# Kernel tuning notes

Hardware: AMD Instinct MI355X
Metric: run time of the kernel (lower is better)

The kernel has to match this reference:

```python
import jax, jax.numpy as jnp
import numpy as np

B, N, E, H = 32, 512, 256, 8
HD = E // H
EPS = 1e-5

def setup_inputs() -> dict:
    key = jax.random.key(0)
    ks = jax.random.split(key, 10)
    x = jax.random.normal(ks[0], (B, N, E), dtype=jnp.float32)
    # boolean masks: True = masked out. Keep diagonal unmasked so no row is fully masked.
    pre = jax.random.bernoulli(ks[1], 0.1, (B, H, N, N))
    eye = jnp.eye(N, dtype=bool)
    pre_mask = jnp.where(eye[None, None, :, :], False, pre)
    post_attn_mask = jax.random.bernoulli(ks[2], 0.1, (B, N))
    s = 1.0 / np.sqrt(E)
    in_proj_w = jax.random.uniform(ks[3], (3 * E, E), jnp.float32, -s, s)
    in_proj_b = jnp.zeros((3 * E,), jnp.float32)
    out_w = jax.random.uniform(ks[4], (E, E), jnp.float32, -s, s)
    out_b = jnp.zeros((E,), jnp.float32)
    gamma = jnp.ones((E,), jnp.float32)
    beta = jnp.zeros((E,), jnp.float32)
    return {"x": x, "pre_mask": pre_mask, "post_attn_mask": post_attn_mask,
            "in_proj_w": in_proj_w, "in_proj_b": in_proj_b,
            "out_w": out_w, "out_b": out_b, "gamma": gamma, "beta": beta}

def reference(x, pre_mask, post_attn_mask, in_proj_w, in_proj_b, out_w, out_b, gamma, beta):
    b, n, e = x.shape
    # fused qkv projection (matches nn.MultiheadAttention in_proj)
    qkv = x @ in_proj_w.T + in_proj_b            # [B,N,3E]
    q, k, v = jnp.split(qkv, 3, axis=-1)
    def heads(t):
        return t.reshape(b, n, H, HD).transpose(0, 2, 1, 3)  # [B,H,N,HD]
    q, k, v = heads(q), heads(k), heads(v)
    scores = jnp.einsum('bhqd,bhkd->bhqk', q * (HD ** -0.5), k)  # [B,H,N,N]
    scores = jnp.where(pre_mask, -1e9, scores)
    w = jax.nn.softmax(scores, axis=-1)                          # [B,H,N,N]
    o = jnp.einsum('bhqk,bhkd->bhqd', w, v)                      # [B,H,N,HD]
    o = o.transpose(0, 2, 1, 3).reshape(b, n, e)
    o = o @ out_w.T + out_b
    # post-attention mask: zero outputs of unavailable agents
    o = jnp.where(post_attn_mask[:, :, None], 0.0, o)
    # residual + LayerNorm
    y = x + o
    mu = y.mean(axis=-1, keepdims=True)
    var = y.var(axis=-1, keepdims=True)
    out = (y - mu) * jax.lax.rsqrt(var + EPS) * gamma + beta
    # attn_weights averaged over heads (PyTorch default average_attn_weights=True)
    attn_weights = w.mean(axis=1)                                # [B,N,N]
    return (out, attn_weights)
```

## Files before the change

### kernel.cpp

```cpp
#include <hip/hip_runtime.h>

#define BB 32
#define NN 512
#define EE 256
#define HH 8
#define HDD 32

typedef __attribute__((ext_vector_type(4))) float f32x4;
typedef __attribute__((ext_vector_type(8))) short s16x8;
typedef unsigned short ushort_t;
typedef unsigned int uint_t;

__device__ __forceinline__ ushort_t f2bf(float f) {
  union { float f; uint_t u; } v; v.f = f;
  uint_t r = v.u + 0x7fffu + ((v.u >> 16) & 1u);
  return (ushort_t)(r >> 16);
}
__device__ __forceinline__ uint_t pk2(float a, float b) {
  return (uint_t)f2bf(a) | ((uint_t)f2bf(b) << 16);
}

__global__ __launch_bounds__(256) void qkv_mfma(
    const float* __restrict__ x, const float* __restrict__ w,
    const float* __restrict__ bias,
    ushort_t* __restrict__ Q, ushort_t* __restrict__ K, ushort_t* __restrict__ V) {
  __shared__ ushort_t sA[128][40];
  __shared__ ushort_t sB[128][40];
  int t = threadIdx.x;
  int bj = blockIdx.x % 6, bm = blockIdx.x / 6;
  int m0 = bm * 128, j0 = bj * 128;
  int w4 = t >> 6, lane = t & 63, quad = lane >> 4, l16 = lane & 15;
  int wy = w4 >> 1, wx = w4 & 1;
  f32x4 acc[4][4];
  #pragma unroll
  for (int a = 0; a < 4; a++)
    #pragma unroll
    for (int b = 0; b < 4; b++) acc[a][b] = (f32x4){0.f, 0.f, 0.f, 0.f};
  int sr = t >> 3, sc = t & 7;
  for (int kk = 0; kk < 256; kk += 32) {
    __syncthreads();
    #pragma unroll
    for (int i = 0; i < 4; i++) {
      int r = sr + 32 * i;
      float4 av = *(const float4*)&x[(size_t)(m0 + r) * 256 + kk + sc * 4];
      float4 bv = *(const float4*)&w[(size_t)(j0 + r) * 256 + kk + sc * 4];
      uint2 pa; pa.x = pk2(av.x, av.y); pa.y = pk2(av.z, av.w);
      uint2 pb; pb.x = pk2(bv.x, bv.y); pb.y = pk2(bv.z, bv.w);
      *(uint2*)&sA[r][sc * 4] = pa;
      *(uint2*)&sB[r][sc * 4] = pb;
    }
    __syncthreads();
    s16x8 af[4], bf[4];
    #pragma unroll
    for (int mt = 0; mt < 4; mt++)
      af[mt] = *(const s16x8*)&sA[wy * 64 + mt * 16 + l16][quad * 8];
    #pragma unroll
    for (int jt = 0; jt < 4; jt++)
      bf[jt] = *(const s16x8*)&sB[wx * 64 + jt * 16 + l16][quad * 8];
    #pragma unroll
    for (int mt = 0; mt < 4; mt++)
      #pragma unroll
      for (int jt = 0; jt < 4; jt++)
        acc[mt][jt] = __builtin_amdgcn_mfma_f32_16x16x32_bf16(af[mt], bf[jt], acc[mt][jt], 0, 0, 0);
  }
  #pragma unroll
  for (int jt = 0; jt < 4; jt++) {
    int j = j0 + wx * 64 + jt * 16 + l16;
    int which = j >> 8, e0 = j & 255, h = e0 >> 5, d0 = e0 & 31;
    ushort_t* dst = (which == 0) ? Q : ((which == 1) ? K : V);
    float b = bias[j];
    #pragma unroll
    for (int mt = 0; mt < 4; mt++) {
      #pragma unroll
      for (int r = 0; r < 4; r++) {
        int m = m0 + wy * 64 + mt * 16 + quad * 4 + r;
        int bi = m >> 9, n = m & 511;
        dst[((size_t)(bi * 8 + h) * 512 + n) * 32 + d0] = f2bf(acc[mt][jt][r] + b);
      }
    }
  }
}

__global__ __launch_bounds__(256) void attn_kernel(
    const ushort_t* __restrict__ Q, const ushort_t* __restrict__ K,
    const ushort_t* __restrict__ V, const int* __restrict__ pre_mask,
    ushort_t* __restrict__ O, float* __restrict__ attnw) {
  __shared__ ushort_t sQ[16 * 32];
  __shared__ ushort_t sP[16 * 520];
  __shared__ float sSum[4][16];
  __shared__ float sO[4][16 * 32];

  int t = threadIdx.x;
  int bb = blockIdx.x >> 5;
  int q0 = (blockIdx.x & 31) << 4;
  int w = t >> 6;
  int lane = t & 63;
  int quad = lane >> 4;
  int l16 = lane & 15;
  int kbase = w * 128;
  const float scale = 0.17677669529663687f;

  float wmean[4][8];
  #pragma unroll
  for (int i = 0; i < 4; i++)
    #pragma unroll
    for (int j = 0; j < 8; j++) wmean[i][j] = 0.f;

  for (int h = 0; h < 8; h++) {
    size_t base = ((size_t)(bb * 8 + h) * 512) * 32;
    const ushort_t* Kg = K + base;
    const ushort_t* Vg = V + base;
    const int* mbase = pre_mask + ((size_t)(bb * 8 + h) * 512 + q0) * 512;

    if (t < 64) {
      ((s16x8*)sQ)[t] = ((const s16x8*)(Q + base + (size_t)q0 * 32))[t];
    }
    __syncthreads();

    s16x8 afrag = *(const s16x8*)&sQ[l16 * 32 + quad * 8];
    float ev[8][4];
    #pragma unroll
    for (int t8 = 0; t8 < 8; t8++) {
      int n0 = kbase + t8 * 16;
      s16x8 bfrag = *(const s16x8*)&Kg[(size_t)(n0 + l16) * 32 + quad * 8];
      f32x4 acc = {0.f, 0.f, 0.f, 0.f};
      acc = __builtin_amdgcn_mfma_f32_16x16x32_bf16(afrag, bfrag, acc, 0, 0, 0);
      #pragma unroll
      for (int i = 0; i < 4; i++) {
        int msk = mbase[(quad * 4 + i) * 512 + n0 + l16];
        ev[t8][i] = msk ? 0.f : __expf(acc[i] * scale);
      }
    }
    float ps[4];
    #pragma unroll
    for (int i = 0; i < 4; i++) {
      float s = 0.f;
      #pragma unroll
      for (int t8 = 0; t8 < 8; t8++) s += ev[t8][i];
      s += __shfl_xor(s, 1, 64);
      s += __shfl_xor(s, 2, 64);
      s += __shfl_xor(s, 4, 64);
      s += __shfl_xor(s, 8, 64);
      ps[i] = s;
    }
    if (l16 == 0) {
      #pragma unroll
      for (int i = 0; i < 4; i++) sSum[w][quad * 4 + i] = ps[i];
    }
    #pragma unroll
    for (int t8 = 0; t8 < 8; t8++)
      #pragma unroll
      for (int i = 0; i < 4; i++)
        sP[(quad * 4 + i) * 520 + kbase + t8 * 16 + l16] = f2bf(ev[t8][i]);
    __syncthreads();

    float inv[4];
    #pragma unroll
    for (int i = 0; i < 4; i++) {
      int r = quad * 4 + i;
      inv[i] = 1.0f / (sSum[0][r] + sSum[1][r] + sSum[2][r] + sSum[3][r]);
    }
    #pragma unroll
    for (int t8 = 0; t8 < 8; t8++)
      #pragma unroll
      for (int i = 0; i < 4; i++)
        wmean[i][t8] += 0.125f * ev[t8][i] * inv[i];

    f32x4 oacc[2];
    oacc[0] = (f32x4){0.f, 0.f, 0.f, 0.f};
    oacc[1] = (f32x4){0.f, 0.f, 0.f, 0.f};
    #pragma unroll
    for (int ks = 0; ks < 4; ks++) {
      s16x8 pa = *(const s16x8*)&sP[l16 * 520 + kbase + ks * 32 + quad * 8];
      #pragma unroll
      for (int dt = 0; dt < 2; dt++) {
        s16x8 vb;
        #pragma unroll
        for (int j = 0; j < 8; j++)
          vb[j] = (short)Vg[(size_t)(kbase + ks * 32 + quad * 8 + j) * 32 + dt * 16 + l16];
        oacc[dt] = __builtin_amdgcn_mfma_f32_16x16x32_bf16(pa, vb, oacc[dt], 0, 0, 0);
      }
    }
    #pragma unroll
    for (int dt = 0; dt < 2; dt++)
      #pragma unroll
      for (int i = 0; i < 4; i++)
        sO[w][(quad * 4 + i) * 32 + dt * 16 + l16] = oacc[dt][i];
    __syncthreads();

    {
      int r = t >> 4;
      int c = (t & 15) * 2;
      float s0 = sO[0][r * 32 + c] + sO[1][r * 32 + c] + sO[2][r * 32 + c] + sO[3][r * 32 + c];
      float s1 = sO[0][r * 32 + c + 1] + sO[1][r * 32 + c + 1] + sO[2][r * 32 + c + 1] + sO[3][r * 32 + c + 1];
      float invr = 1.0f / (sSum[0][r] + sSum[1][r] + sSum[2][r] + sSum[3][r]);
      uint_t pk = pk2(s0 * invr, s1 * invr);
      *(uint_t*)&O[((size_t)(bb * 512 + q0 + r) * 256) + h * 32 + c] = pk;
    }
  }

  float* arow = attnw + (size_t)(bb * 512 + q0) * 512;
  #pragma unroll
  for (int i = 0; i < 4; i++)
    #pragma unroll
    for (int t8 = 0; t8 < 8; t8++)
      arow[(quad * 4 + i) * 512 + kbase + t8 * 16 + l16] = wmean[i][t8];
}

__global__ __launch_bounds__(256) void proj_ln_mfma(
    const ushort_t* __restrict__ O, const float* __restrict__ x,
    const float* __restrict__ w, const float* __restrict__ bias,
    const int* __restrict__ post_mask,
    const float* __restrict__ gamma, const float* __restrict__ beta,
    float* __restrict__ out) {
  __shared__ ushort_t sB[256][40];
  int t = threadIdx.x;
  int m0 = blockIdx.x * 64;
  int w4 = t >> 6, lane = t & 63, quad = lane >> 4, l16 = lane & 15;
  int mrow0 = m0 + w4 * 16;
  f32x4 acc[16];
  #pragma unroll
  for (int jt = 0; jt < 16; jt++) acc[jt] = (f32x4){0.f, 0.f, 0.f, 0.f};
  int sr = t >> 3, sc = t & 7;
  for (int kk = 0; kk < 256; kk += 32) {
    __syncthreads();
    #pragma unroll
    for (int i = 0; i < 8; i++) {
      int r = sr + 32 * i;
      float4 bv = *(const float4*)&w[(size_t)r * 256 + kk + sc * 4];
      uint2 pb; pb.x = pk2(bv.x, bv.y); pb.y = pk2(bv.z, bv.w);
      *(uint2*)&sB[r][sc * 4] = pb;
    }
    __syncthreads();
    s16x8 af = *(const s16x8*)&O[(size_t)(mrow0 + l16) * 256 + kk + quad * 8];
    #pragma unroll
    for (int jt = 0; jt < 16; jt++) {
      s16x8 bf = *(const s16x8*)&sB[jt * 16 + l16][quad * 8];
      acc[jt] = __builtin_amdgcn_mfma_f32_16x16x32_bf16(af, bf, acc[jt], 0, 0, 0);
    }
  }
  #pragma unroll
  for (int i = 0; i < 4; i++) {
    int m = mrow0 + quad * 4 + i;
    int bi = m >> 9, n = m & 511;
    bool msk = post_mask[bi * 512 + n] != 0;
    float y[16];
    float s1 = 0.f, s2 = 0.f;
    #pragma unroll
    for (int jt = 0; jt < 16; jt++) {
      int j = jt * 16 + l16;
      float p = msk ? 0.f : (acc[jt][i] + bias[j]);
      float yy = x[(size_t)m * 256 + j] + p;
      y[jt] = yy; s1 += yy; s2 += yy * yy;
    }
    s1 += __shfl_xor(s1, 1, 64); s1 += __shfl_xor(s1, 2, 64);
    s1 += __shfl_xor(s1, 4, 64); s1 += __shfl_xor(s1, 8, 64);
    s2 += __shfl_xor(s2, 1, 64); s2 += __shfl_xor(s2, 2, 64);
    s2 += __shfl_xor(s2, 4, 64); s2 += __shfl_xor(s2, 8, 64);
    float mu = s1 * (1.0f / 256.0f);
    float var = s2 * (1.0f / 256.0f) - mu * mu;
    float rstd = rsqrtf(var + 1e-5f);
    #pragma unroll
    for (int jt = 0; jt < 16; jt++) {
      int j = jt * 16 + l16;
      out[(size_t)m * 256 + j] = (y[jt] - mu) * rstd * gamma[j] + beta[j];
    }
  }
}

extern "C" void kernel_launch(void* const* d_in, const int* in_sizes, int n_in,
                              void* d_out, int out_size, void* d_ws, size_t ws_size,
                              hipStream_t stream) {
  const float* x       = (const float*)d_in[0];
  const int*   pre_m   = (const int*)d_in[1];
  const int*   post_m  = (const int*)d_in[2];
  const float* in_w    = (const float*)d_in[3];
  const float* in_b    = (const float*)d_in[4];
  const float* out_w   = (const float*)d_in[5];
  const float* out_b   = (const float*)d_in[6];
  const float* gamma   = (const float*)d_in[7];
  const float* beta    = (const float*)d_in[8];
  float* out   = (float*)d_out;
  float* attnw = out + (size_t)BB * NN * EE;
  ushort_t* Q = (ushort_t*)d_ws;
  ushort_t* K = Q + (size_t)BB * HH * NN * HDD;
  ushort_t* V = K + (size_t)BB * HH * NN * HDD;
  ushort_t* O = V + (size_t)BB * HH * NN * HDD;

  qkv_mfma<<<dim3(768), dim3(256), 0, stream>>>(x, in_w, in_b, Q, K, V);
  attn_kernel<<<dim3(1024), dim3(256), 0, stream>>>(Q, K, V, pre_m, O, attnw);
  proj_ln_mfma<<<dim3(256), dim3(256), 0, stream>>>(O, x, out_w, out_b, post_m, gamma, beta, out);
}
```

Before: 503.6 us.

## Pre-convert inputs to bf16 and store V transposed for vectorized PV loads

Adds a conversion kernel that turns x and both weight matrices into bf16 once, so the GEMM kernels load 16-byte bf16 vectors instead of converting fp32 per tile. The QKV kernel now writes V transposed (head-dim major), which lets the attention kernel load each V fragment with one 16-byte read instead of eight strided scalar reads. The cost is three extra launches, additional workspace traffic for the bf16 copies, and more scattered stores when writing V transposed.

```diff
diff --git a/kernel.cpp b/kernel.cpp
--- a/kernel.cpp
+++ b/kernel.cpp
@@ -20,10 +20,20 @@
   return (uint_t)f2bf(a) | ((uint_t)f2bf(b) << 16);
 }
 
+__global__ __launch_bounds__(256) void cvt_bf16(
+    const float* __restrict__ src, ushort_t* __restrict__ dst, int n4) {
+  int i = blockIdx.x * 256 + threadIdx.x;
+  if (i < n4) {
+    float4 v = ((const float4*)src)[i];
+    uint2 p; p.x = pk2(v.x, v.y); p.y = pk2(v.z, v.w);
+    ((uint2*)dst)[i] = p;
+  }
+}
+
 __global__ __launch_bounds__(256) void qkv_mfma(
-    const float* __restrict__ x, const float* __restrict__ w,
+    const ushort_t* __restrict__ xb, const ushort_t* __restrict__ wb,
     const float* __restrict__ bias,
-    ushort_t* __restrict__ Q, ushort_t* __restrict__ K, ushort_t* __restrict__ V) {
+    ushort_t* __restrict__ Q, ushort_t* __restrict__ K, ushort_t* __restrict__ Vt) {
   __shared__ ushort_t sA[128][40];
   __shared__ ushort_t sB[128][40];
   int t = threadIdx.x;
@@ -36,18 +46,14 @@
   for (int a = 0; a < 4; a++)
     #pragma unroll
     for (int b = 0; b < 4; b++) acc[a][b] = (f32x4){0.f, 0.f, 0.f, 0.f};
-  int sr = t >> 3, sc = t & 7;
+  int sr2 = t >> 2, sc2 = (t & 3) * 8;
   for (int kk = 0; kk < 256; kk += 32) {
     __syncthreads();
     #pragma unroll
-    for (int i = 0; i < 4; i++) {
-      int r = sr + 32 * i;
-      float4 av = *(const float4*)&x[(size_t)(m0 + r) * 256 + kk + sc * 4];
-      float4 bv = *(const float4*)&w[(size_t)(j0 + r) * 256 + kk + sc * 4];
-      uint2 pa; pa.x = pk2(av.x, av.y); pa.y = pk2(av.z, av.w);
-      uint2 pb; pb.x = pk2(bv.x, bv.y); pb.y = pk2(bv.z, bv.w);
-      *(uint2*)&sA[r][sc * 4] = pa;
-      *(uint2*)&sB[r][sc * 4] = pb;
+    for (int p = 0; p < 2; p++) {
+      int r = sr2 + 64 * p;
+      *(s16x8*)&sA[r][sc2] = *(const s16x8*)&xb[(size_t)(m0 + r) * 256 + kk + sc2];
+      *(s16x8*)&sB[r][sc2] = *(const s16x8*)&wb[(size_t)(j0 + r) * 256 + kk + sc2];
     }
     __syncthreads();
     s16x8 af[4], bf[4];
@@ -67,7 +73,6 @@
   for (int jt = 0; jt < 4; jt++) {
     int j = j0 + wx * 64 + jt * 16 + l16;
     int which = j >> 8, e0 = j & 255, h = e0 >> 5, d0 = e0 & 31;
-    ushort_t* dst = (which == 0) ? Q : ((which == 1) ? K : V);
     float b = bias[j];
     #pragma unroll
     for (int mt = 0; mt < 4; mt++) {
@@ -75,7 +80,13 @@
       for (int r = 0; r < 4; r++) {
         int m = m0 + wy * 64 + mt * 16 + quad * 4 + r;
         int bi = m >> 9, n = m & 511;
-        dst[((size_t)(bi * 8 + h) * 512 + n) * 32 + d0] = f2bf(acc[mt][jt][r] + b);
+        ushort_t val = f2bf(acc[mt][jt][r] + b);
+        if (which == 2) {
+          Vt[((size_t)(bi * 8 + h) * 32 + d0) * 512 + n] = val;
+        } else {
+          ushort_t* dst = (which == 0) ? Q : K;
+          dst[((size_t)(bi * 8 + h) * 512 + n) * 32 + d0] = val;
+        }
       }
     }
   }
@@ -83,7 +94,7 @@
 
 __global__ __launch_bounds__(256) void attn_kernel(
     const ushort_t* __restrict__ Q, const ushort_t* __restrict__ K,
-    const ushort_t* __restrict__ V, const int* __restrict__ pre_mask,
+    const ushort_t* __restrict__ Vt, const int* __restrict__ pre_mask,
     ushort_t* __restrict__ O, float* __restrict__ attnw) {
   __shared__ ushort_t sQ[16 * 32];
   __shared__ ushort_t sP[16 * 520];
@@ -109,7 +120,7 @@
   for (int h = 0; h < 8; h++) {
     size_t base = ((size_t)(bb * 8 + h) * 512) * 32;
     const ushort_t* Kg = K + base;
-    const ushort_t* Vg = V + base;
+    const ushort_t* Vg = Vt + base;
     const int* mbase = pre_mask + ((size_t)(bb * 8 + h) * 512 + q0) * 512;
 
     if (t < 64) {
@@ -174,10 +185,7 @@
       s16x8 pa = *(const s16x8*)&sP[l16 * 520 + kbase + ks * 32 + quad * 8];
       #pragma unroll
       for (int dt = 0; dt < 2; dt++) {
-        s16x8 vb;
-        #pragma unroll
-        for (int j = 0; j < 8; j++)
-          vb[j] = (short)Vg[(size_t)(kbase + ks * 32 + quad * 8 + j) * 32 + dt * 16 + l16];
+        s16x8 vb = *(const s16x8*)&Vg[(size_t)(dt * 16 + l16) * 512 + kbase + ks * 32 + quad * 8];
         oacc[dt] = __builtin_amdgcn_mfma_f32_16x16x32_bf16(pa, vb, oacc[dt], 0, 0, 0);
       }
     }
@@ -209,7 +217,7 @@
 
 __global__ __launch_bounds__(256) void proj_ln_mfma(
     const ushort_t* __restrict__ O, const float* __restrict__ x,
-    const float* __restrict__ w, const float* __restrict__ bias,
+    const ushort_t* __restrict__ wb, const float* __restrict__ bias,
     const int* __restrict__ post_mask,
     const float* __restrict__ gamma, const float* __restrict__ beta,
     float* __restrict__ out) {
@@ -221,15 +229,13 @@
   f32x4 acc[16];
   #pragma unroll
   for (int jt = 0; jt < 16; jt++) acc[jt] = (f32x4){0.f, 0.f, 0.f, 0.f};
-  int sr = t >> 3, sc = t & 7;
+  int sr2 = t >> 2, sc2 = (t & 3) * 8;
   for (int kk = 0; kk < 256; kk += 32) {
     __syncthreads();
     #pragma unroll
-    for (int i = 0; i < 8; i++) {
-      int r = sr + 32 * i;
-      float4 bv = *(const float4*)&w[(size_t)r * 256 + kk + sc * 4];
-      uint2 pb; pb.x = pk2(bv.x, bv.y); pb.y = pk2(bv.z, bv.w);
-      *(uint2*)&sB[r][sc * 4] = pb;
+    for (int p = 0; p < 4; p++) {
+      int r = sr2 + 64 * p;
+      *(s16x8*)&sB[r][sc2] = *(const s16x8*)&wb[(size_t)r * 256 + kk + sc2];
     }
     __syncthreads();
     s16x8 af = *(const s16x8*)&O[(size_t)(mrow0 + l16) * 256 + kk + quad * 8];
@@ -282,12 +288,18 @@
   const float* beta    = (const float*)d_in[8];
   float* out   = (float*)d_out;
   float* attnw = out + (size_t)BB * NN * EE;
-  ushort_t* Q = (ushort_t*)d_ws;
-  ushort_t* K = Q + (size_t)BB * HH * NN * HDD;
-  ushort_t* V = K + (size_t)BB * HH * NN * HDD;
-  ushort_t* O = V + (size_t)BB * HH * NN * HDD;
-
-  qkv_mfma<<<dim3(768), dim3(256), 0, stream>>>(x, in_w, in_b, Q, K, V);
-  attn_kernel<<<dim3(1024), dim3(256), 0, stream>>>(Q, K, V, pre_m, O, attnw);
-  proj_ln_mfma<<<dim3(256), dim3(256), 0, stream>>>(O, x, out_w, out_b, post_m, gamma, beta, out);
-}
+  ushort_t* Q  = (ushort_t*)d_ws;
+  ushort_t* K  = Q  + (size_t)BB * HH * NN * HDD;
+  ushort_t* Vt = K  + (size_t)BB * HH * NN * HDD;
+  ushort_t* O  = Vt + (size_t)BB * HH * NN * HDD;
+  ushort_t* xb  = O  + (size_t)BB * NN * EE;
+  ushort_t* wib = xb + (size_t)BB * NN * EE;
+  ushort_t* wob = wib + (size_t)3 * EE * EE;
+
+  cvt_bf16<<<dim3(4096), dim3(256), 0, stream>>>(x, xb, BB * NN * EE / 4);
+  cvt_bf16<<<dim3(192), dim3(256), 0, stream>>>(in_w, wib, 3 * EE * EE / 4);
+  cvt_bf16<<<dim3(64), dim3(256), 0, stream>>>(out_w, wob, EE * EE / 4);
+  qkv_mfma<<<dim3(768), dim3(256), 0, stream>>>(xb, wib, in_b, Q, K, Vt);
+  attn_kernel<<<dim3(1024), dim3(256), 0, stream>>>(Q, K, Vt, pre_m, O, attnw);
+  proj_ln_mfma<<<dim3(256), dim3(256), 0, stream>>>(O, x, wob, out_b, post_m, gamma, beta, out);
+}
```

After: 486.4 us. 3.4% less time.
